# Optimization experiments

Measured on AMD Instinct MI355X. Metric: run time of the kernel, lower is better.

The kernel has to match this reference:

```python
import jax, jax.numpy as jnp
import numpy as np

N_BINS = 15
N_SAMPLES = 2_000_000
N_CLASSES = 128


def setup_inputs() -> dict:
    key = jax.random.key(0)
    k1, k2 = jax.random.split(key)
    probs = jax.random.normal(k1, (N_SAMPLES, N_CLASSES), dtype=jnp.float32)
    labels = jax.random.randint(k2, (N_SAMPLES,), 0, N_CLASSES, dtype=jnp.int64 if jax.config.read('jax_enable_x64') else jnp.int32)
    return {"probs": probs, "labels": labels, "is_logit": 1}


def reference(probs, labels, is_logit):
    if is_logit:
        probs = jax.nn.softmax(probs, axis=-1)
    # confidences / predictions / accuracies
    confidences = jnp.max(probs, axis=1)                      # [N]
    predictions = jnp.argmax(probs, axis=1)                   # [N]
    accuracies = (predictions == labels).astype(probs.dtype)  # [N]

    # bin index for half-open bins (lower, upper]: conf in ((i)/B, (i+1)/B]
    # ceil(conf * B) - 1 maps conf==upper to bin i; clip handles conf<=0 edge.
    bin_idx = jnp.clip(jnp.ceil(confidences * N_BINS).astype(jnp.int32) - 1, 0, N_BINS - 1)

    counts = jax.ops.segment_sum(jnp.ones_like(confidences), bin_idx, num_segments=N_BINS)
    conf_sum = jax.ops.segment_sum(confidences, bin_idx, num_segments=N_BINS)
    acc_sum = jax.ops.segment_sum(accuracies, bin_idx, num_segments=N_BINS)

    n = confidences.shape[0]
    safe = jnp.maximum(counts, 1.0)
    gap = jnp.abs(conf_sum / safe - acc_sum / safe)           # [N_BINS]
    prop = counts / n                                         # [N_BINS]
    ece = jnp.sum(jnp.where(counts > 0, gap * prop, 0.0))
    return ece.reshape(1)
```

## Files before the change

### kernel.cpp

```cpp
#include <hip/hip_runtime.h>

#define N_BINS 15
#define BLOCKS 2048

__global__ __launch_bounds__(256) void ece_main(
    const float* __restrict__ probs,
    const int* __restrict__ labels,
    const int* __restrict__ is_logit_p,
    float* __restrict__ bins,
    int n_rows)
{
    __shared__ float s_count[N_BINS];
    __shared__ float s_conf[N_BINS];
    __shared__ float s_acc[N_BINS];

    const int tid = threadIdx.x;
    if (tid < N_BINS) { s_count[tid] = 0.f; s_conf[tid] = 0.f; s_acc[tid] = 0.f; }
    __syncthreads();

    const int is_logit = *is_logit_p;
    const int lane = tid & 63;
    const int sub  = lane & 7;
    const int grp  = tid >> 3;

    long long row = (long long)blockIdx.x * 32 + grp;
    const long long stride = (long long)gridDim.x * 32;

    for (; row < n_rows; row += stride) {
        const float4* rp = (const float4*)(probs + (size_t)row * 128);
        const float4 v0 = rp[sub];
        const float4 v1 = rp[sub + 8];
        const float4 v2 = rp[sub + 16];
        const float4 v3 = rp[sub + 24];
        const int label = labels[row];

        float m = fmaxf(fmaxf(fmaxf(v0.x, v0.y), fmaxf(v0.z, v0.w)),
                        fmaxf(fmaxf(v1.x, v1.y), fmaxf(v1.z, v1.w)));
        m = fmaxf(m, fmaxf(fmaxf(fmaxf(v2.x, v2.y), fmaxf(v2.z, v2.w)),
                           fmaxf(fmaxf(v3.x, v3.y), fmaxf(v3.z, v3.w))));
        m = fmaxf(m, __shfl_xor(m, 1, 64));
        m = fmaxf(m, __shfl_xor(m, 2, 64));
        m = fmaxf(m, __shfl_xor(m, 4, 64));

        float conf;
        if (is_logit) {
            float s = __expf(v0.x - m) + __expf(v0.y - m)
                    + __expf(v0.z - m) + __expf(v0.w - m)
                    + __expf(v1.x - m) + __expf(v1.y - m)
                    + __expf(v1.z - m) + __expf(v1.w - m)
                    + __expf(v2.x - m) + __expf(v2.y - m)
                    + __expf(v2.z - m) + __expf(v2.w - m)
                    + __expf(v3.x - m) + __expf(v3.y - m)
                    + __expf(v3.z - m) + __expf(v3.w - m);
            s += __shfl_xor(s, 1, 64);
            s += __shfl_xor(s, 2, 64);
            s += __shfl_xor(s, 4, 64);
            conf = 1.0f / s;
        } else {
            conf = m;
        }

        const int f = label >> 2;
        const int c = label & 3;
        const int k = f >> 3;
        float4 vk = (k == 0) ? v0 : (k == 1) ? v1 : (k == 2) ? v2 : v3;
        float lv = (c == 0) ? vk.x : (c == 1) ? vk.y : (c == 2) ? vk.z : vk.w;
        const bool mine = ((f & 7) == sub) && (lv == m);
        const unsigned long long bal = __ballot(mine);

        if (sub == 0) {
            int bin = (int)ceilf(conf * (float)N_BINS) - 1;
            bin = bin < 0 ? 0 : (bin > N_BINS - 1 ? N_BINS - 1 : bin);
            const float acc = ((bal >> (lane & 56)) & 0xFFull) ? 1.0f : 0.0f;
            atomicAdd(&s_count[bin], 1.0f);
            atomicAdd(&s_conf[bin],  conf);
            atomicAdd(&s_acc[bin],   acc);
        }
    }

    __syncthreads();
    if (tid < N_BINS) {
        atomicAdd(&bins[tid],            s_count[tid]);
        atomicAdd(&bins[N_BINS + tid],   s_conf[tid]);
        atomicAdd(&bins[2*N_BINS + tid], s_acc[tid]);
    }
}

__global__ void ece_final(const float* __restrict__ bins,
                          float* __restrict__ out, int n_rows)
{
    if (threadIdx.x == 0 && blockIdx.x == 0) {
        float ece = 0.f;
        for (int i = 0; i < N_BINS; ++i) {
            float c = bins[i];
            if (c > 0.f) {
                float gap = fabsf(bins[N_BINS + i] / c - bins[2*N_BINS + i] / c);
                ece += gap * (c / (float)n_rows);
            }
        }
        out[0] = ece;
    }
}

extern "C" void kernel_launch(void* const* d_in, const int* in_sizes, int n_in,
                              void* d_out, int out_size, void* d_ws, size_t ws_size,
                              hipStream_t stream) {
    const float* probs    = (const float*)d_in[0];
    const int*   labels   = (const int*)d_in[1];
    const int*   is_logit = (const int*)d_in[2];
    float*       out      = (float*)d_out;
    float*       bins     = (float*)d_ws;
    const int n_rows = in_sizes[1];

    hipMemsetAsync(bins, 0, 3 * N_BINS * sizeof(float), stream);
    ece_main<<<BLOCKS, 256, 0, stream>>>(probs, labels, is_logit, bins, n_rows);
    ece_final<<<1, 64, 0, stream>>>(bins, out, n_rows);
}
```

Before: 1.271 ms.

## Software-prefetch next row with nontemporal loads and per-wave shared bins

```diff
diff --git a/kernel.cpp b/kernel.cpp
--- a/kernel.cpp
+++ b/kernel.cpp
@@ -1,7 +1,13 @@
 #include <hip/hip_runtime.h>
 
 #define N_BINS 15
-#define BLOCKS 2048
+#define BLOCKS 1024
+
+typedef float f4 __attribute__((ext_vector_type(4)));
+
+__device__ __forceinline__ float max4(f4 v) {
+    return fmaxf(fmaxf(v[0], v[1]), fmaxf(v[2], v[3]));
+}
 
 __global__ __launch_bounds__(256) void ece_main(
     const float* __restrict__ probs,
@@ -10,48 +16,65 @@
     float* __restrict__ bins,
     int n_rows)
 {
-    __shared__ float s_count[N_BINS];
-    __shared__ float s_conf[N_BINS];
-    __shared__ float s_acc[N_BINS];
+    __shared__ float s_bins[4][3][17];
 
     const int tid = threadIdx.x;
-    if (tid < N_BINS) { s_count[tid] = 0.f; s_conf[tid] = 0.f; s_acc[tid] = 0.f; }
+    if (tid < 4 * 3 * 17) ((float*)s_bins)[tid] = 0.f;
     __syncthreads();
 
     const int is_logit = *is_logit_p;
     const int lane = tid & 63;
-    const int sub  = lane & 7;
+    const int wave = tid >> 6;
+    const int sub  = tid & 7;
     const int grp  = tid >> 3;
 
     long long row = (long long)blockIdx.x * 32 + grp;
     const long long stride = (long long)gridDim.x * 32;
+    const size_t pstep = (size_t)stride * 32;
 
-    for (; row < n_rows; row += stride) {
-        const float4* rp = (const float4*)(probs + (size_t)row * 128);
-        const float4 v0 = rp[sub];
-        const float4 v1 = rp[sub + 8];
-        const float4 v2 = rp[sub + 16];
-        const float4 v3 = rp[sub + 24];
-        const int label = labels[row];
+    const f4* rp = (const f4*)probs + (size_t)row * 32 + sub;
 
-        float m = fmaxf(fmaxf(fmaxf(v0.x, v0.y), fmaxf(v0.z, v0.w)),
-                        fmaxf(fmaxf(v1.x, v1.y), fmaxf(v1.z, v1.w)));
-        m = fmaxf(m, fmaxf(fmaxf(fmaxf(v2.x, v2.y), fmaxf(v2.z, v2.w)),
-                           fmaxf(fmaxf(v3.x, v3.y), fmaxf(v3.z, v3.w))));
+    f4 a0, a1, a2, a3;
+    int lab = 0;
+    bool valid = row < n_rows;
+    if (valid) {
+        a0 = __builtin_nontemporal_load(rp);
+        a1 = __builtin_nontemporal_load(rp + 8);
+        a2 = __builtin_nontemporal_load(rp + 16);
+        a3 = __builtin_nontemporal_load(rp + 24);
+        lab = labels[row];
+    }
+
+    while (valid) {
+        const long long nrow = row + stride;
+        const bool nvalid = nrow < n_rows;
+        const f4* np = rp + pstep;
+        f4 b0, b1, b2, b3;
+        int nlab = 0;
+        if (nvalid) {
+            b0 = __builtin_nontemporal_load(np);
+            b1 = __builtin_nontemporal_load(np + 8);
+            b2 = __builtin_nontemporal_load(np + 16);
+            b3 = __builtin_nontemporal_load(np + 24);
+            nlab = labels[nrow];
+        }
+
+        float m = fmaxf(fmaxf(max4(a0), max4(a1)), fmaxf(max4(a2), max4(a3)));
         m = fmaxf(m, __shfl_xor(m, 1, 64));
         m = fmaxf(m, __shfl_xor(m, 2, 64));
         m = fmaxf(m, __shfl_xor(m, 4, 64));
 
         float conf;
         if (is_logit) {
-            float s = __expf(v0.x - m) + __expf(v0.y - m)
-                    + __expf(v0.z - m) + __expf(v0.w - m)
-                    + __expf(v1.x - m) + __expf(v1.y - m)
-                    + __expf(v1.z - m) + __expf(v1.w - m)
-                    + __expf(v2.x - m) + __expf(v2.y - m)
-                    + __expf(v2.z - m) + __expf(v2.w - m)
-                    + __expf(v3.x - m) + __expf(v3.y - m)
-                    + __expf(v3.z - m) + __expf(v3.w - m);
+            float e0 = (__expf(a0[0] - m) + __expf(a0[1] - m))
+                     + (__expf(a0[2] - m) + __expf(a0[3] - m));
+            float e1 = (__expf(a1[0] - m) + __expf(a1[1] - m))
+                     + (__expf(a1[2] - m) + __expf(a1[3] - m));
+            float e2 = (__expf(a2[0] - m) + __expf(a2[1] - m))
+                     + (__expf(a2[2] - m) + __expf(a2[3] - m));
+            float e3 = (__expf(a3[0] - m) + __expf(a3[1] - m))
+                     + (__expf(a3[2] - m) + __expf(a3[3] - m));
+            float s = (e0 + e1) + (e2 + e3);
             s += __shfl_xor(s, 1, 64);
             s += __shfl_xor(s, 2, 64);
             s += __shfl_xor(s, 4, 64);
@@ -60,11 +83,11 @@
             conf = m;
         }
 
-        const int f = label >> 2;
-        const int c = label & 3;
+        const int f = lab >> 2;
+        const int c = lab & 3;
         const int k = f >> 3;
-        float4 vk = (k == 0) ? v0 : (k == 1) ? v1 : (k == 2) ? v2 : v3;
-        float lv = (c == 0) ? vk.x : (c == 1) ? vk.y : (c == 2) ? vk.z : vk.w;
+        f4 vk = (k == 0) ? a0 : (k == 1) ? a1 : (k == 2) ? a2 : a3;
+        float lv = (c == 0) ? vk[0] : (c == 1) ? vk[1] : (c == 2) ? vk[2] : vk[3];
         const bool mine = ((f & 7) == sub) && (lv == m);
         const unsigned long long bal = __ballot(mine);
 
@@ -72,17 +95,21 @@
             int bin = (int)ceilf(conf * (float)N_BINS) - 1;
             bin = bin < 0 ? 0 : (bin > N_BINS - 1 ? N_BINS - 1 : bin);
             const float acc = ((bal >> (lane & 56)) & 0xFFull) ? 1.0f : 0.0f;
-            atomicAdd(&s_count[bin], 1.0f);
-            atomicAdd(&s_conf[bin],  conf);
-            atomicAdd(&s_acc[bin],   acc);
+            atomicAdd(&s_bins[wave][0][bin], 1.0f);
+            atomicAdd(&s_bins[wave][1][bin], conf);
+            atomicAdd(&s_bins[wave][2][bin], acc);
         }
+
+        row = nrow; valid = nvalid; rp = np;
+        a0 = b0; a1 = b1; a2 = b2; a3 = b3; lab = nlab;
     }
 
     __syncthreads();
-    if (tid < N_BINS) {
-        atomicAdd(&bins[tid],            s_count[tid]);
-        atomicAdd(&bins[N_BINS + tid],   s_conf[tid]);
-        atomicAdd(&bins[2*N_BINS + tid], s_acc[tid]);
+    if (tid < 3 * N_BINS) {
+        const int c = tid / N_BINS;
+        const int b = tid - c * N_BINS;
+        atomicAdd(&bins[tid], s_bins[0][c][b] + s_bins[1][c][b]
+                            + s_bins[2][c][b] + s_bins[3][c][b]);
     }
 }
 
@@ -94,7 +121,7 @@
         for (int i = 0; i < N_BINS; ++i) {
             float c = bins[i];
             if (c > 0.f) {
-                float gap = fabsf(bins[N_BINS + i] / c - bins[2*N_BINS + i] / c);
+                float gap = fabsf(bins[N_BINS + i] / c - bins[2 * N_BINS + i] / c);
                 ece += gap * (c / (float)n_rows);
             }
         }
```

New measurement: 1.236 ms. 1.03x faster.
